# Kernel tuning notes

Measured on AMD Instinct MI355X. Metric: run time of the kernel, lower is better.

## Reference

```python
import jax, jax.numpy as jnp
import numpy as np

N_NODES = 50000
N_EDGES = 800000
D_MODEL = 128
N_LAYERS = 3


def setup_inputs() -> dict:
    key = jax.random.key(0)
    k1, k2, k3 = jax.random.split(key, 3)
    in_feat = jax.random.normal(k1, (N_NODES, D_MODEL), dtype=jnp.float32)
    edge_index = jax.random.randint(k2, (2, N_EDGES), 0, N_NODES, dtype=jnp.int64)
    # per-layer GraphConv weights (Glorot-ish scale) and biases
    Ws = jax.random.normal(k3, (N_LAYERS, D_MODEL, D_MODEL), dtype=jnp.float32) / np.sqrt(D_MODEL)
    bs = jnp.zeros((N_LAYERS, D_MODEL), dtype=jnp.float32)
    return {"in_feat": in_feat, "edge_index": edge_index, "Ws": Ws, "bs": bs}


def _degrees(edge_index, num_nodes):
    src, dst = edge_index[0], edge_index[1]
    ones = jnp.ones(src.shape[0], dtype=jnp.float32)
    out_deg = jax.ops.segment_sum(ones, src, num_segments=num_nodes)
    in_deg = jax.ops.segment_sum(ones, dst, num_segments=num_nodes)
    # DGL GraphConv norm='both': deg^{-1/2}, clamp zero-degree to 1
    out_norm = jax.lax.rsqrt(jnp.maximum(out_deg, 1.0))
    in_norm = jax.lax.rsqrt(jnp.maximum(in_deg, 1.0))
    return out_norm, in_norm


def reference(in_feat, edge_index, Ws, bs):
    src, dst = edge_index[0], edge_index[1]
    num_nodes = in_feat.shape[0]
    out_norm, in_norm = _degrees(edge_index, num_nodes)

    h = in_feat
    for i in range(N_LAYERS):
        # symmetric normalization: D_out^{-1/2} on source side
        hs = h * out_norm[:, None]
        # gather messages along edges and sum-aggregate into destinations
        msgs = hs[src]                                   # [E, d]
        agg = jax.ops.segment_sum(msgs, dst, num_segments=num_nodes)  # [N, d]
        agg = agg * in_norm[:, None]                     # D_in^{-1/2} on dest side
        h = agg @ Ws[i] + bs[i]
    return h
```

## Files before the change

kernel.cpp:

```cpp
#include <hip/hip_runtime.h>


#define NN 50000
#define NE 800000
#define DM 128
#define NB 196
#define NGB 12500
#define CHN 12500
#define NCOP 32
#define NFB 782

typedef unsigned short u16;
typedef __attribute__((ext_vector_type(8))) short bf16x8;
typedef __attribute__((ext_vector_type(4))) float f32x4;

#define FMA4(av, sv, wv) \
  av.x += (sv) * (wv).x; av.y += (sv) * (wv).y; av.z += (sv) * (wv).z; av.w += (sv) * (wv).w;

__device__ __forceinline__ float bf2f(u16 u) {
  return __uint_as_float((unsigned)u << 16);
}
__device__ __forceinline__ u16 f2bf(float f) {
  unsigned x = __float_as_uint(f);
  return (u16)((x + 0x7fffu + ((x >> 16) & 1u)) >> 16);
}
__device__ __forceinline__ float4 bf4(ushort4 u) {
  return make_float4(bf2f(u.x), bf2f(u.y), bf2f(u.z), bf2f(u.w));
}

__global__ void k_hist(const int* __restrict__ src, const int* __restrict__ dst,
                       int* __restrict__ hcop) {
  __shared__ int h[CHN];
  int b = blockIdx.x;
  int arr   = b >> 7;
  int chunk = (b >> 5) & 3;
  int copy  = b & 31;
  const int* idx = arr ? dst : src;
  int lo = chunk * CHN;
  for (int i = threadIdx.x; i < CHN; i += 256) h[i] = 0;
  __syncthreads();
  const int4* e4 = reinterpret_cast<const int4*>(idx) + copy * (NE / 4 / NCOP);
  for (int i = threadIdx.x; i < NE / 4 / NCOP; i += 256) {
    int4 v = e4[i];
    unsigned a;
    a = (unsigned)(v.x - lo); if (a < (unsigned)CHN) atomicAdd(&h[a], 1);
    a = (unsigned)(v.y - lo); if (a < (unsigned)CHN) atomicAdd(&h[a], 1);
    a = (unsigned)(v.z - lo); if (a < (unsigned)CHN) atomicAdd(&h[a], 1);
    a = (unsigned)(v.w - lo); if (a < (unsigned)CHN) atomicAdd(&h[a], 1);
  }
  __syncthreads();
  int* o = hcop + (size_t)b * CHN;
  for (int i = threadIdx.x; i < CHN; i += 256) o[i] = h[i];
}

__global__ void k_scan_part(const int* __restrict__ hcop, int* __restrict__ co,
                            int* __restrict__ ci, int* __restrict__ bsum) {
  __shared__ int s[256];
  int i = blockIdx.x * 256 + threadIdx.x;
  int sco = 0, sci = 0;
  if (i < NN) {
    int ch = i / CHN;
    int loc = i - ch * CHN;
    const int* pco = hcop + (size_t)(ch * 32) * CHN + loc;
    const int* pci = hcop + (size_t)(128 + ch * 32) * CHN + loc;
#pragma unroll
    for (int p = 0; p < NCOP; ++p) {
      sco += pco[(size_t)p * CHN];
      sci += pci[(size_t)p * CHN];
    }
    co[i] = sco;
    ci[i] = sci;
  }
  s[threadIdx.x] = sci;
  __syncthreads();
  for (int off = 128; off > 0; off >>= 1) {
    if (threadIdx.x < off) s[threadIdx.x] += s[threadIdx.x + off];
    __syncthreads();
  }
  if (threadIdx.x == 0) bsum[blockIdx.x] = s[0];
}

__global__ void k_scan_out2(const int* __restrict__ ci, const int* __restrict__ co,
                            const int* __restrict__ bsum, int* __restrict__ rowptr,
                            float* __restrict__ onorm, float* __restrict__ inorm,
                            const int* __restrict__ hcop_dst, int* __restrict__ pcur) {
  __shared__ int s[256];
  int t = threadIdx.x;
  int bv = (t < NB) ? bsum[t] : 0;
  s[t] = bv;
  __syncthreads();
  for (int off = 1; off < 256; off <<= 1) {
    int u = (t >= off) ? s[t - off] : 0;
    __syncthreads();
    s[t] += u;
    __syncthreads();
  }
  int boff_blk = s[blockIdx.x] - bsum[blockIdx.x];
  __syncthreads();

  int i = blockIdx.x * 256 + t;
  int v = (i < NN) ? ci[i] : 0;
  s[t] = v;
  __syncthreads();
  for (int off = 1; off < 256; off <<= 1) {
    int u = (t >= off) ? s[t - off] : 0;
    __syncthreads();
    s[t] += u;
    __syncthreads();
  }
  if (i < NN) {
    int ex = boff_blk + s[t] - v;
    rowptr[i] = ex;
    onorm[i] = rsqrtf(fmaxf((float)co[i], 1.0f));
    inorm[i] = rsqrtf(fmaxf((float)v, 1.0f));
    int ch = i / CHN;
    int loc = i - ch * CHN;
    const int* hb = hcop_dst + (size_t)(ch * 32) * CHN + loc;
    int* pb = pcur + (size_t)(ch * 32) * CHN + loc;
    int run = ex;
#pragma unroll
    for (int p = 0; p < NCOP; ++p) {
      pb[(size_t)p * CHN] = run;
      run += hb[(size_t)p * CHN];
    }
  }
  if (blockIdx.x == 0 && t == 0) rowptr[NN] = NE;
}

__global__ void k_fill2(const int* __restrict__ src, const int* __restrict__ dst,
                        const int* __restrict__ pcur, int* __restrict__ col,
                        const float* __restrict__ feat, u16* __restrict__ featb) {
  __shared__ int cur[CHN];
  int b = blockIdx.x;
  if (b >= 128) {
    size_t base = ((size_t)(b - 128) * 256 + threadIdx.x) * 8;
    const size_t stride = (size_t)NFB * 256 * 8;
#pragma unroll
    for (int it = 0; it < 4; ++it, base += stride) {
      if (base < (size_t)NN * DM) {
        float4 f0 = *reinterpret_cast<const float4*>(feat + base);
        float4 f1 = *reinterpret_cast<const float4*>(feat + base + 4);
        ushort4 u0 = make_ushort4(f2bf(f0.x), f2bf(f0.y), f2bf(f0.z), f2bf(f0.w));
        ushort4 u1 = make_ushort4(f2bf(f1.x), f2bf(f1.y), f2bf(f1.z), f2bf(f1.w));
        *reinterpret_cast<ushort4*>(featb + base) = u0;
        *reinterpret_cast<ushort4*>(featb + base + 4) = u1;
      }
    }
    return;
  }
  int chunk = b >> 5;
  int copy  = b & 31;
  int lo = chunk * CHN;
  const int* pc = pcur + (size_t)b * CHN;
  for (int i = threadIdx.x; i < CHN; i += 256) cur[i] = pc[i];
  __syncthreads();
  const int4* s4 = reinterpret_cast<const int4*>(src) + copy * (NE / 4 / NCOP);
  const int4* d4 = reinterpret_cast<const int4*>(dst) + copy * (NE / 4 / NCOP);
  for (int i = threadIdx.x; i < NE / 4 / NCOP; i += 256) {
    int4 s = s4[i];
    int4 d = d4[i];
    unsigned a;
    int p;
    a = (unsigned)(d.x - lo); if (a < (unsigned)CHN) { p = atomicAdd(&cur[a], 1); col[p] = s.x; }
    a = (unsigned)(d.y - lo); if (a < (unsigned)CHN) { p = atomicAdd(&cur[a], 1); col[p] = s.y; }
    a = (unsigned)(d.z - lo); if (a < (unsigned)CHN) { p = atomicAdd(&cur[a], 1); col[p] = s.z; }
    a = (unsigned)(d.w - lo); if (a < (unsigned)CHN) { p = atomicAdd(&cur[a], 1); col[p] = s.w; }
  }
}

template <int VMODE, int EXTRA, int OUTMODE>
__global__ void k_gather_t(const u16* __restrict__ h, const int* __restrict__ rowptr,
                           const int* __restrict__ col, const float* __restrict__ onorm,
                           const float* __restrict__ inorm, const float* __restrict__ vin,
                           u16* __restrict__ aggb, float* __restrict__ outf,
                           float* __restrict__ vout,
                           const float* __restrict__ mA, const float* __restrict__ mB,
                           float* __restrict__ mCf, u16* __restrict__ mCt,
                           const float* __restrict__ vb1, const float* __restrict__ vB1,
                           float* __restrict__ vc1,
                           const float* __restrict__ vb2, const float* __restrict__ vB2,
                           float* __restrict__ vc2,
                           const float* __restrict__ pv1, const float* __restrict__ pv2,
                           const float* __restrict__ pc1, const float* __restrict__ pc2,
                           const float* __restrict__ pb3) {
  if (EXTRA) {
    int eb = (int)blockIdx.x - NGB;
    if (eb >= 0) {
      if (eb < 64) {
        int i0 = eb * 2 + (threadIdx.x >> 7);
        int j = threadIdx.x & 127;
        float acc = 0.f;
        for (int k = 0; k < DM; ++k) acc += mA[i0 * DM + k] * mB[k * DM + j];
        if (EXTRA == 1) mCf[i0 * DM + j] = acc;
        else            mCt[j * DM + i0] = f2bf(acc);
      } else if (EXTRA == 2) {
        int t = threadIdx.x;
        if (t < DM) {
          float acc = 0.f;
          for (int k = 0; k < DM; ++k) acc += vb1[k] * vB1[k * DM + t];
          vc1[t] = acc;
        } else {
          int j = t - DM;
          float acc = 0.f;
          for (int k = 0; k < DM; ++k) acc += vb2[k] * vB2[k * DM + j];
          vc2[j] = acc;
        }
      }
      return;
    }
  }
  int tid = blockIdx.x * blockDim.x + threadIdx.x;
  int n = tid >> 6;
  if (n >= NN) return;
  int half = (threadIdx.x >> 5) & 1;
  int l32 = threadIdx.x & 31;
  int beg = rowptr[n], end = rowptr[n + 1];
  const ushort4* h4 = reinterpret_cast<const ushort4*>(h);
  float4 a0 = make_float4(0.f, 0.f, 0.f, 0.f);
  float4 a1 = make_float4(0.f, 0.f, 0.f, 0.f);
  float4 a2 = make_float4(0.f, 0.f, 0.f, 0.f);
  float4 a3 = make_float4(0.f, 0.f, 0.f, 0.f);
  float av = 0.f;
  int e = beg + half;
  for (; e + 6 < end; e += 8) {
    int s0 = col[e], s1 = col[e + 2], s2 = col[e + 4], s3 = col[e + 6];
    float n0 = onorm[s0], n1 = onorm[s1], n2 = onorm[s2], n3 = onorm[s3];
    float4 v0 = bf4(h4[(size_t)s0 * 32 + l32]);
    float4 v1 = bf4(h4[(size_t)s1 * 32 + l32]);
    float4 v2 = bf4(h4[(size_t)s2 * 32 + l32]);
    float4 v3 = bf4(h4[(size_t)s3 * 32 + l32]);
    if (VMODE == 1) av += n0 + n1 + n2 + n3;
    if (VMODE == 2) av += n0 * vin[s0] + n1 * vin[s1] + n2 * vin[s2] + n3 * vin[s3];
    FMA4(a0, n0, v0)
    FMA4(a1, n1, v1)
    FMA4(a2, n2, v2)
    FMA4(a3, n3, v3)
  }
  for (; e < end; e += 2) {
    int s0 = col[e];
    float n0 = onorm[s0];
    float4 v0 = bf4(h4[(size_t)s0 * 32 + l32]);
    if (VMODE == 1) av += n0;
    if (VMODE == 2) av += n0 * vin[s0];
    FMA4(a0, n0, v0)
  }
  a0.x += a1.x + a2.x + a3.x;
  a0.y += a1.y + a2.y + a3.y;
  a0.z += a1.z + a2.z + a3.z;
  a0.w += a1.w + a2.w + a3.w;
  a0.x += __shfl_xor(a0.x, 32);
  a0.y += __shfl_xor(a0.y, 32);
  a0.z += __shfl_xor(a0.z, 32);
  a0.w += __shfl_xor(a0.w, 32);
  if (VMODE) av += __shfl_xor(av, 32);
  if (half == 0) {
    float sc = inorm[n];
    float4 o = make_float4(a0.x * sc, a0.y * sc, a0.z * sc, a0.w * sc);
    if (OUTMODE == 0) {
      reinterpret_cast<ushort4*>(aggb)[(size_t)n * 32 + l32] =
          make_ushort4(f2bf(o.x), f2bf(o.y), f2bf(o.z), f2bf(o.w));
    } else {
      int jc = l32 * 4;
      float4 e1 = *reinterpret_cast<const float4*>(pc1 + jc);
      float4 e2 = *reinterpret_cast<const float4*>(pc2 + jc);
      float4 e3 = *reinterpret_cast<const float4*>(pb3 + jc);
      float q1 = pv1[n], q2 = pv2[n];
      o.x += q2 * e1.x + q1 * e2.x + e3.x;
      o.y += q2 * e1.y + q1 * e2.y + e3.y;
      o.z += q2 * e1.z + q1 * e2.z + e3.z;
      o.w += q2 * e1.w + q1 * e2.w + e3.w;
      reinterpret_cast<float4*>(outf)[(size_t)n * 32 + l32] = o;
    }
    if (VMODE && l32 == 0) vout[n] = av * sc;
  }
}

__launch_bounds__(256, 4)
__global__ void k_gemm_mfma(const u16* __restrict__ A, const u16* __restrict__ Bt,
                            u16* __restrict__ T) {
  int w = threadIdx.x >> 6;
  int l = threadIdx.x & 63;
  int rbase = blockIdx.x * 32 + 16 * (w & 1);
  int jb0   = 64 * (w >> 1);
  int row = rbase + (l & 15);
  int rr = row < NN ? row : NN - 1;
  int kg = (l >> 4) * 8;
  const short* As = reinterpret_cast<const short*>(A);
  const short* Bs = reinterpret_cast<const short*>(Bt);
  bf16x8 fa0 = *reinterpret_cast<const bf16x8*>(As + (size_t)rr * DM + 0 * 32 + kg);
  bf16x8 fa1 = *reinterpret_cast<const bf16x8*>(As + (size_t)rr * DM + 1 * 32 + kg);
  bf16x8 fa2 = *reinterpret_cast<const bf16x8*>(As + (size_t)rr * DM + 2 * 32 + kg);
  bf16x8 fa3 = *reinterpret_cast<const bf16x8*>(As + (size_t)rr * DM + 3 * 32 + kg);
#pragma unroll
  for (int ct = 0; ct < 4; ++ct) {
    int jb = jb0 + ct * 16;
    const short* bp = Bs + (size_t)(jb + (l & 15)) * DM + kg;
    bf16x8 fb0 = *reinterpret_cast<const bf16x8*>(bp + 0 * 32);
    bf16x8 fb1 = *reinterpret_cast<const bf16x8*>(bp + 1 * 32);
    bf16x8 fb2 = *reinterpret_cast<const bf16x8*>(bp + 2 * 32);
    bf16x8 fb3 = *reinterpret_cast<const bf16x8*>(bp + 3 * 32);
    f32x4 c = {0.f, 0.f, 0.f, 0.f};
    c = __builtin_amdgcn_mfma_f32_16x16x32_bf16(fa0, fb0, c, 0, 0, 0);
    c = __builtin_amdgcn_mfma_f32_16x16x32_bf16(fa1, fb1, c, 0, 0, 0);
    c = __builtin_amdgcn_mfma_f32_16x16x32_bf16(fa2, fb2, c, 0, 0, 0);
    c = __builtin_amdgcn_mfma_f32_16x16x32_bf16(fa3, fb3, c, 0, 0, 0);
    int orow = rbase + (l >> 4) * 4;
    int ocol = jb + (l & 15);
#pragma unroll
    for (int r = 0; r < 4; ++r) {
      if (orow + r < NN) T[(size_t)(orow + r) * DM + ocol] = f2bf(c[r]);
    }
  }
}

extern "C" void kernel_launch(void* const* d_in, const int* in_sizes, int n_in,
                              void* d_out, int out_size, void* d_ws, size_t ws_size,
                              hipStream_t stream) {
  const float* in_feat = (const float*)d_in[0];
  const int*   ei      = (const int*)d_in[1];
  const float* Ws      = (const float*)d_in[2];
  const float* bs      = (const float*)d_in[3];
  float* out = (float*)d_out;

  const int* src = ei;
  const int* dst = ei + NE;
  const float* W1 = Ws;
  const float* W2 = Ws + DM * DM;
  const float* W3 = Ws + 2 * DM * DM;
  const float* b1 = bs;
  const float* b2 = bs + DM;
  const float* b3 = bs + 2 * DM;

  char* w = (char*)d_ws;
  int* hcop   = (int*)w;            w += (size_t)256 * CHN * sizeof(int);
  int* co     = (int*)w;            w += NN * sizeof(int);
  int* ci     = (int*)w;            w += NN * sizeof(int);
  int* rowptr = (int*)w;            w += (NN + 1) * sizeof(int);
  int* bsum   = (int*)w;            w += NB * sizeof(int);
  int* col    = (int*)w;            w += NE * sizeof(int);
  float* onorm = (float*)w;         w += NN * sizeof(float);
  float* inorm = (float*)w;         w += NN * sizeof(float);
  float* v1    = (float*)w;         w += NN * sizeof(float);
  float* v2    = (float*)w;         w += NN * sizeof(float);
  float* W23   = (float*)w;         w += DM * DM * sizeof(float);
  u16*   W123t = (u16*)w;           w += DM * DM * sizeof(u16);
  float* c1    = (float*)w;         w += DM * sizeof(float);
  float* c2    = (float*)w;         w += DM * sizeof(float);
  u16* featb  = (u16*)w;            w += (size_t)NN * DM * sizeof(u16);
  u16* g1b    = (u16*)w;            w += (size_t)NN * DM * sizeof(u16);
  u16* g2b    = (u16*)w;            w += (size_t)NN * DM * sizeof(u16);
  u16* tb     = (u16*)w;            w += (size_t)NN * DM * sizeof(u16);

  int* pcur = hcop;
  const int* hcop_dst = hcop + (size_t)128 * CHN;

  k_hist<<<256, 256, 0, stream>>>(src, dst, hcop);
  k_scan_part<<<NB, 256, 0, stream>>>(hcop, co, ci, bsum);
  k_scan_out2<<<NB, 256, 0, stream>>>(ci, co, bsum, rowptr, onorm, inorm, hcop_dst, pcur);
  k_fill2<<<128 + NFB, 256, 0, stream>>>(src, dst, pcur, col, in_feat, featb);

  k_gather_t<1, 1, 0><<<NGB + 64, 256, 0, stream>>>(featb, rowptr, col, onorm, inorm,
                                                    nullptr, g1b, nullptr, v1,
                                                    W2, W3, W23, nullptr,
                                                    nullptr, nullptr, nullptr,
                                                    nullptr, nullptr, nullptr,
                                                    nullptr, nullptr, nullptr, nullptr, nullptr);
  k_gather_t<2, 2, 0><<<NGB + 65, 256, 0, stream>>>(g1b, rowptr, col, onorm, inorm,
                                                    v1, g2b, nullptr, v2,
                                                    W1, W23, nullptr, W123t,
                                                    b1, W23, c1, b2, W3, c2,
                                                    nullptr, nullptr, nullptr, nullptr, nullptr);
  k_gemm_mfma<<<(NN + 31) / 32, 256, 0, stream>>>(g2b, W123t, tb);
  k_gather_t<0, 0, 1><<<NGB, 256, 0, stream>>>(tb, rowptr, col, onorm, inorm,
                                               nullptr, nullptr, out, nullptr,
                                               nullptr, nullptr, nullptr, nullptr,
                                               nullptr, nullptr, nullptr,
                                               nullptr, nullptr, nullptr,
                                               v1, v2, c1, c2, b3);
}
```

Measured before the change: 204.0 us.

## Widen gather loads to 16B per lane and move bf16 conversion into scan kernel

The gather kernel now has 16 lanes per node row, each loading 8 bf16 values as one int4, with four edge groups per wavefront instead of two halves loading 4 values each. The wider loads are meant to cut load instructions per edge and raise memory-level parallelism on the random row gathers, at the cost of a longer shuffle reduction and fewer independent accumulators. The feature-to-bf16 conversion blocks move from the fill kernel into the scan-partial kernel so they overlap a lighter stage. The workspace is also reordered so the large bf16 buffers sit at aligned offsets.

```diff
diff --git a/kernel.cpp b/kernel.cpp
--- a/kernel.cpp
+++ b/kernel.cpp
@@ -14,9 +14,6 @@
 typedef __attribute__((ext_vector_type(8))) short bf16x8;
 typedef __attribute__((ext_vector_type(4))) float f32x4;
 
-#define FMA4(av, sv, wv) \
-  av.x += (sv) * (wv).x; av.y += (sv) * (wv).y; av.z += (sv) * (wv).z; av.w += (sv) * (wv).w;
-
 __device__ __forceinline__ float bf2f(u16 u) {
   return __uint_as_float((unsigned)u << 16);
 }
@@ -24,9 +21,8 @@
   unsigned x = __float_as_uint(f);
   return (u16)((x + 0x7fffu + ((x >> 16) & 1u)) >> 16);
 }
-__device__ __forceinline__ float4 bf4(ushort4 u) {
-  return make_float4(bf2f(u.x), bf2f(u.y), bf2f(u.z), bf2f(u.w));
-}
+__device__ __forceinline__ float bflo(int u) { return __int_as_float(u << 16); }
+__device__ __forceinline__ float bfhi(int u) { return __int_as_float(u & 0xffff0000); }
 
 __global__ void k_hist(const int* __restrict__ src, const int* __restrict__ dst,
                        int* __restrict__ hcop) {
@@ -54,9 +50,27 @@
 }
 
 __global__ void k_scan_part(const int* __restrict__ hcop, int* __restrict__ co,
-                            int* __restrict__ ci, int* __restrict__ bsum) {
+                            int* __restrict__ ci, int* __restrict__ bsum,
+                            const float* __restrict__ feat, u16* __restrict__ featb) {
   __shared__ int s[256];
-  int i = blockIdx.x * 256 + threadIdx.x;
+  int b = blockIdx.x;
+  if (b >= NB) {
+    size_t base = ((size_t)(b - NB) * 256 + threadIdx.x) * 8;
+    const size_t stride = (size_t)NFB * 256 * 8;
+#pragma unroll
+    for (int it = 0; it < 4; ++it, base += stride) {
+      if (base < (size_t)NN * DM) {
+        float4 f0 = *reinterpret_cast<const float4*>(feat + base);
+        float4 f1 = *reinterpret_cast<const float4*>(feat + base + 4);
+        ushort4 u0 = make_ushort4(f2bf(f0.x), f2bf(f0.y), f2bf(f0.z), f2bf(f0.w));
+        ushort4 u1 = make_ushort4(f2bf(f1.x), f2bf(f1.y), f2bf(f1.z), f2bf(f1.w));
+        *reinterpret_cast<ushort4*>(featb + base) = u0;
+        *reinterpret_cast<ushort4*>(featb + base + 4) = u1;
+      }
+    }
+    return;
+  }
+  int i = b * 256 + threadIdx.x;
   int sco = 0, sci = 0;
   if (i < NN) {
     int ch = i / CHN;
@@ -77,7 +91,7 @@
     if (threadIdx.x < off) s[threadIdx.x] += s[threadIdx.x + off];
     __syncthreads();
   }
-  if (threadIdx.x == 0) bsum[blockIdx.x] = s[0];
+  if (threadIdx.x == 0) bsum[b] = s[0];
 }
 
 __global__ void k_scan_out2(const int* __restrict__ ci, const int* __restrict__ co,
@@ -128,29 +142,11 @@
 }
 
 __global__ void k_fill2(const int* __restrict__ src, const int* __restrict__ dst,
-                        const int* __restrict__ pcur, int* __restrict__ col,
-                        const float* __restrict__ feat, u16* __restrict__ featb) {
+                        const int* __restrict__ pcur, int* __restrict__ col) {
   __shared__ int cur[CHN];
   int b = blockIdx.x;
-  if (b >= 128) {
-    size_t base = ((size_t)(b - 128) * 256 + threadIdx.x) * 8;
-    const size_t stride = (size_t)NFB * 256 * 8;
-#pragma unroll
-    for (int it = 0; it < 4; ++it, base += stride) {
-      if (base < (size_t)NN * DM) {
-        float4 f0 = *reinterpret_cast<const float4*>(feat + base);
-        float4 f1 = *reinterpret_cast<const float4*>(feat + base + 4);
-        ushort4 u0 = make_ushort4(f2bf(f0.x), f2bf(f0.y), f2bf(f0.z), f2bf(f0.w));
-        ushort4 u1 = make_ushort4(f2bf(f1.x), f2bf(f1.y), f2bf(f1.z), f2bf(f1.w));
-        *reinterpret_cast<ushort4*>(featb + base) = u0;
-        *reinterpret_cast<ushort4*>(featb + base + 4) = u1;
-      }
-    }
-    return;
-  }
-  int chunk = b >> 5;
   int copy  = b & 31;
-  int lo = chunk * CHN;
+  int lo = (b >> 5) * CHN;
   const int* pc = pcur + (size_t)b * CHN;
   for (int i = threadIdx.x; i < CHN; i += 256) cur[i] = pc[i];
   __syncthreads();
@@ -167,6 +163,12 @@
     a = (unsigned)(d.w - lo); if (a < (unsigned)CHN) { p = atomicAdd(&cur[a], 1); col[p] = s.w; }
   }
 }
+
+#define ACC8(uu, nn)                     \
+  aa.x += (nn) * bflo((uu).x); ab.x += (nn) * bfhi((uu).x); \
+  aa.y += (nn) * bflo((uu).y); ab.y += (nn) * bfhi((uu).y); \
+  aa.z += (nn) * bflo((uu).z); ab.z += (nn) * bfhi((uu).z); \
+  aa.w += (nn) * bflo((uu).w); ab.w += (nn) * bfhi((uu).w);
 
 template <int VMODE, int EXTRA, int OUTMODE>
 __global__ void k_gather_t(const u16* __restrict__ h, const int* __restrict__ rowptr,
@@ -212,66 +214,74 @@
   int tid = blockIdx.x * blockDim.x + threadIdx.x;
   int n = tid >> 6;
   if (n >= NN) return;
-  int half = (threadIdx.x >> 5) & 1;
-  int l32 = threadIdx.x & 31;
+  int g   = (threadIdx.x >> 4) & 3;
+  int l16 = threadIdx.x & 15;
   int beg = rowptr[n], end = rowptr[n + 1];
-  const ushort4* h4 = reinterpret_cast<const ushort4*>(h);
-  float4 a0 = make_float4(0.f, 0.f, 0.f, 0.f);
-  float4 a1 = make_float4(0.f, 0.f, 0.f, 0.f);
-  float4 a2 = make_float4(0.f, 0.f, 0.f, 0.f);
-  float4 a3 = make_float4(0.f, 0.f, 0.f, 0.f);
+  const int4* h16 = reinterpret_cast<const int4*>(h);
+  float4 aa = make_float4(0.f, 0.f, 0.f, 0.f);
+  float4 ab = make_float4(0.f, 0.f, 0.f, 0.f);
   float av = 0.f;
-  int e = beg + half;
-  for (; e + 6 < end; e += 8) {
-    int s0 = col[e], s1 = col[e + 2], s2 = col[e + 4], s3 = col[e + 6];
-    float n0 = onorm[s0], n1 = onorm[s1], n2 = onorm[s2], n3 = onorm[s3];
-    float4 v0 = bf4(h4[(size_t)s0 * 32 + l32]);
-    float4 v1 = bf4(h4[(size_t)s1 * 32 + l32]);
-    float4 v2 = bf4(h4[(size_t)s2 * 32 + l32]);
-    float4 v3 = bf4(h4[(size_t)s3 * 32 + l32]);
-    if (VMODE == 1) av += n0 + n1 + n2 + n3;
-    if (VMODE == 2) av += n0 * vin[s0] + n1 * vin[s1] + n2 * vin[s2] + n3 * vin[s3];
-    FMA4(a0, n0, v0)
-    FMA4(a1, n1, v1)
-    FMA4(a2, n2, v2)
-    FMA4(a3, n3, v3)
-  }
-  for (; e < end; e += 2) {
+  int e = beg + g;
+  for (; e + 4 < end; e += 8) {
+    int s0 = col[e], s1 = col[e + 4];
+    float n0 = onorm[s0], n1 = onorm[s1];
+    int4 u0 = h16[(size_t)s0 * 16 + l16];
+    int4 u1 = h16[(size_t)s1 * 16 + l16];
+    if (VMODE == 1) av += n0 + n1;
+    if (VMODE == 2) av += n0 * vin[s0] + n1 * vin[s1];
+    ACC8(u0, n0)
+    ACC8(u1, n1)
+  }
+  for (; e < end; e += 4) {
     int s0 = col[e];
     float n0 = onorm[s0];
-    float4 v0 = bf4(h4[(size_t)s0 * 32 + l32]);
+    int4 u0 = h16[(size_t)s0 * 16 + l16];
     if (VMODE == 1) av += n0;
     if (VMODE == 2) av += n0 * vin[s0];
-    FMA4(a0, n0, v0)
-  }
-  a0.x += a1.x + a2.x + a3.x;
-  a0.y += a1.y + a2.y + a3.y;
-  a0.z += a1.z + a2.z + a3.z;
-  a0.w += a1.w + a2.w + a3.w;
-  a0.x += __shfl_xor(a0.x, 32);
-  a0.y += __shfl_xor(a0.y, 32);
-  a0.z += __shfl_xor(a0.z, 32);
-  a0.w += __shfl_xor(a0.w, 32);
-  if (VMODE) av += __shfl_xor(av, 32);
-  if (half == 0) {
+    ACC8(u0, n0)
+  }
+  aa.x += __shfl_xor(aa.x, 16); aa.y += __shfl_xor(aa.y, 16);
+  aa.z += __shfl_xor(aa.z, 16); aa.w += __shfl_xor(aa.w, 16);
+  ab.x += __shfl_xor(ab.x, 16); ab.y += __shfl_xor(ab.y, 16);
+  ab.z += __shfl_xor(ab.z, 16); ab.w += __shfl_xor(ab.w, 16);
+  aa.x += __shfl_xor(aa.x, 32); aa.y += __shfl_xor(aa.y, 32);
+  aa.z += __shfl_xor(aa.z, 32); aa.w += __shfl_xor(aa.w, 32);
+  ab.x += __shfl_xor(ab.x, 32); ab.y += __shfl_xor(ab.y, 32);
+  ab.z += __shfl_xor(ab.z, 32); ab.w += __shfl_xor(ab.w, 32);
+  if (VMODE) { av += __shfl_xor(av, 16); av += __shfl_xor(av, 32); }
+  if (g == 0) {
     float sc = inorm[n];
-    float4 o = make_float4(a0.x * sc, a0.y * sc, a0.z * sc, a0.w * sc);
+    aa.x *= sc; aa.y *= sc; aa.z *= sc; aa.w *= sc;
+    ab.x *= sc; ab.y *= sc; ab.z *= sc; ab.w *= sc;
     if (OUTMODE == 0) {
-      reinterpret_cast<ushort4*>(aggb)[(size_t)n * 32 + l32] =
-          make_ushort4(f2bf(o.x), f2bf(o.y), f2bf(o.z), f2bf(o.w));
+      int4 o;
+      o.x = ((int)f2bf(ab.x) << 16) | f2bf(aa.x);
+      o.y = ((int)f2bf(ab.y) << 16) | f2bf(aa.y);
+      o.z = ((int)f2bf(ab.z) << 16) | f2bf(aa.z);
+      o.w = ((int)f2bf(ab.w) << 16) | f2bf(aa.w);
+      reinterpret_cast<int4*>(aggb)[(size_t)n * 16 + l16] = o;
     } else {
-      int jc = l32 * 4;
-      float4 e1 = *reinterpret_cast<const float4*>(pc1 + jc);
-      float4 e2 = *reinterpret_cast<const float4*>(pc2 + jc);
-      float4 e3 = *reinterpret_cast<const float4*>(pb3 + jc);
+      int jc = l16 * 8;
+      float4 e1a = *reinterpret_cast<const float4*>(pc1 + jc);
+      float4 e1b = *reinterpret_cast<const float4*>(pc1 + jc + 4);
+      float4 e2a = *reinterpret_cast<const float4*>(pc2 + jc);
+      float4 e2b = *reinterpret_cast<const float4*>(pc2 + jc + 4);
+      float4 e3a = *reinterpret_cast<const float4*>(pb3 + jc);
+      float4 e3b = *reinterpret_cast<const float4*>(pb3 + jc + 4);
       float q1 = pv1[n], q2 = pv2[n];
-      o.x += q2 * e1.x + q1 * e2.x + e3.x;
-      o.y += q2 * e1.y + q1 * e2.y + e3.y;
-      o.z += q2 * e1.z + q1 * e2.z + e3.z;
-      o.w += q2 * e1.w + q1 * e2.w + e3.w;
-      reinterpret_cast<float4*>(outf)[(size_t)n * 32 + l32] = o;
-    }
-    if (VMODE && l32 == 0) vout[n] = av * sc;
+      float4 o0, o1;
+      o0.x = aa.x + q2 * e1a.x + q1 * e2a.x + e3a.x;
+      o0.y = ab.x + q2 * e1a.y + q1 * e2a.y + e3a.y;
+      o0.z = aa.y + q2 * e1a.z + q1 * e2a.z + e3a.z;
+      o0.w = ab.y + q2 * e1a.w + q1 * e2a.w + e3a.w;
+      o1.x = aa.z + q2 * e1b.x + q1 * e2b.x + e3b.x;
+      o1.y = ab.z + q2 * e1b.y + q1 * e2b.y + e3b.y;
+      o1.z = aa.w + q2 * e1b.z + q1 * e2b.z + e3b.z;
+      o1.w = ab.w + q2 * e1b.w + q1 * e2b.w + e3b.w;
+      *reinterpret_cast<float4*>(outf + (size_t)n * DM + jc) = o0;
+      *reinterpret_cast<float4*>(outf + (size_t)n * DM + jc + 4) = o1;
+    }
+    if (VMODE && l16 == 0) vout[n] = av * sc;
   }
 }
 
@@ -333,6 +343,12 @@
 
   char* w = (char*)d_ws;
   int* hcop   = (int*)w;            w += (size_t)256 * CHN * sizeof(int);
+  u16* featb  = (u16*)w;            w += (size_t)NN * DM * sizeof(u16);
+  u16* g1b    = (u16*)w;            w += (size_t)NN * DM * sizeof(u16);
+  u16* g2b    = (u16*)w;            w += (size_t)NN * DM * sizeof(u16);
+  u16* tb     = (u16*)w;            w += (size_t)NN * DM * sizeof(u16);
+  u16* W123t  = (u16*)w;            w += DM * DM * sizeof(u16);
+  float* W23  = (float*)w;          w += DM * DM * sizeof(float);
   int* co     = (int*)w;            w += NN * sizeof(int);
   int* ci     = (int*)w;            w += NN * sizeof(int);
   int* rowptr = (int*)w;            w += (NN + 1) * sizeof(int);
@@ -342,22 +358,16 @@
   float* inorm = (float*)w;         w += NN * sizeof(float);
   float* v1    = (float*)w;         w += NN * sizeof(float);
   float* v2    = (float*)w;         w += NN * sizeof(float);
-  float* W23   = (float*)w;         w += DM * DM * sizeof(float);
-  u16*   W123t = (u16*)w;           w += DM * DM * sizeof(u16);
   float* c1    = (float*)w;         w += DM * sizeof(float);
   float* c2    = (float*)w;         w += DM * sizeof(float);
-  u16* featb  = (u16*)w;            w += (size_t)NN * DM * sizeof(u16);
-  u16* g1b    = (u16*)w;            w += (size_t)NN * DM * sizeof(u16);
-  u16* g2b    = (u16*)w;            w += (size_t)NN * DM * sizeof(u16);
-  u16* tb     = (u16*)w;            w += (size_t)NN * DM * sizeof(u16);
 
   int* pcur = hcop;
   const int* hcop_dst = hcop + (size_t)128 * CHN;
 
   k_hist<<<256, 256, 0, stream>>>(src, dst, hcop);
-  k_scan_part<<<NB, 256, 0, stream>>>(hcop, co, ci, bsum);
+  k_scan_part<<<NB + NFB, 256, 0, stream>>>(hcop, co, ci, bsum, in_feat, featb);
   k_scan_out2<<<NB, 256, 0, stream>>>(ci, co, bsum, rowptr, onorm, inorm, hcop_dst, pcur);
-  k_fill2<<<128 + NFB, 256, 0, stream>>>(src, dst, pcur, col, in_feat, featb);
+  k_fill2<<<128, 256, 0, stream>>>(src, dst, pcur, col);
 
   k_gather_t<1, 1, 0><<<NGB + 64, 256, 0, stream>>>(featb, rowptr, col, onorm, inorm,
                                                     nullptr, g1b, nullptr, v1,
```

Measured after the change: 186.0 us, median of 2. 1.1x faster.
